# Optimization experiments

Measured on AMD Instinct MI355X. Metric: run time of the kernel, lower is better.

Reference implementation:

```python
import jax, jax.numpy as jnp
import numpy as np

N = 50000
E = 800000
D = 128


def setup_inputs() -> dict:
    key = jax.random.key(0)
    ks = jax.random.split(key, 10)
    x = jax.random.normal(ks[0], (N, D), dtype=jnp.float32)
    edge_index = jax.random.randint(ks[1], (2, E), 0, N, dtype=jnp.int32)
    s = 1.0 / np.sqrt(D)
    W1 = jax.random.uniform(ks[2], (D, D), jnp.float32, -s, s)
    b1 = jnp.zeros((D,), jnp.float32)
    W2 = jax.random.uniform(ks[3], (D, D), jnp.float32, -s, s)
    b2 = jnp.zeros((D,), jnp.float32)
    Wt = jax.random.uniform(ks[4], (D, 1), jnp.float32, -s, s)
    bt = jnp.zeros((1,), jnp.float32)
    We = jax.random.uniform(ks[5], (D, 1), jnp.float32, -s, s)
    be = jnp.zeros((1,), jnp.float32)
    return {"x": x, "edge_index": edge_index, "W1": W1, "b1": b1,
            "W2": W2, "b2": b2, "Wt": Wt, "bt": bt, "We": We, "be": be}


def _gcn_norm(edge_index, n):
    # add self-loops, then symmetric normalization D^-1/2 (A+I) D^-1/2
    loop = jnp.arange(n, dtype=edge_index.dtype)
    src = jnp.concatenate([edge_index[0], loop])
    dst = jnp.concatenate([edge_index[1], loop])
    ones = jnp.ones(src.shape[0], dtype=jnp.float32)
    deg = jax.ops.segment_sum(ones, dst, num_segments=n)
    dinv = jnp.where(deg > 0, jax.lax.rsqrt(deg), 0.0)
    norm = dinv[src] * dinv[dst]  # [E+N]
    return src, dst, norm


def _gcn_conv(h, W, b, src, dst, norm, n):
    h = h @ W                                   # [N, D'] dense GEMM
    msg = h[src] * norm[:, None]                # gather + scale
    out = jax.ops.segment_sum(msg, dst, num_segments=n)  # scatter-add
    return out + b


def reference(x, edge_index, W1, b1, W2, b2, Wt, bt, We, be):
    n = x.shape[0]
    src, dst, norm = _gcn_norm(edge_index, n)
    h = jax.nn.relu(_gcn_conv(x, W1, b1, src, dst, norm, n))
    h = jax.nn.relu(_gcn_conv(h, W2, b2, src, dst, norm, n))
    # dropout is identity at inference (eval mode)
    survival_time = h @ Wt + bt   # [N, 1]
    event_status = h @ We + be    # [N, 1]
    return survival_time, event_status
```

## Files before the change

kernel.cpp:

```cpp
#include <hip/hip_runtime.h>
#include <hip/hip_fp16.h>
#include <math.h>

#define NN 50000
#define NE 800000
#define DD 128

#define NB  196
#define CAP 5300
#define EPB 4096
#define A_BLOCKS 196

#define SLAB2 (NN * 64)

typedef _Float16 half8_t __attribute__((ext_vector_type(8)));
typedef float f32x4 __attribute__((ext_vector_type(4)));


__global__ __launch_bounds__(256) void k_setup(const int* __restrict__ src, const int* __restrict__ dst,
                                               int* __restrict__ bcnt, unsigned int* __restrict__ ebuf,
                                               const float* __restrict__ W1, const float* __restrict__ W2,
                                               __half* __restrict__ WT1, __half* __restrict__ WT2) {
    const int blk = blockIdx.x;
    const int tid = threadIdx.x;

    if (blk < A_BLOCKS) {
        __shared__ int hist[256];
        __shared__ int scanbuf[256];
        __shared__ int gbase[256];
        __shared__ unsigned int stage[EPB];
        __shared__ int tgt[EPB];

        const int e0 = blk * EPB;
        int nE = NE - e0; if (nE > EPB) nE = EPB;

        hist[tid] = 0;
        __syncthreads();

        unsigned int pk[16];
        unsigned int br[16];
        #pragma unroll
        for (int j = 0; j < 16; ++j) {
            int idx = tid + j * 256;
            if (idx < nE) {
                int e = e0 + idx;
                int s = src[e], d = dst[e];
                int b = d >> 8;
                int r = atomicAdd(&hist[b], 1);
                pk[j] = (unsigned int)s | ((unsigned int)(d & 255) << 16);
                br[j] = (unsigned int)b | ((unsigned int)r << 8);
            }
        }
        __syncthreads();
        int v = hist[tid];
        scanbuf[tid] = v;
        __syncthreads();
        for (int o = 1; o < 256; o <<= 1) {
            int t2 = (tid >= o) ? scanbuf[tid - o] : 0;
            __syncthreads();
            scanbuf[tid] += t2;
            __syncthreads();
        }
        int base_excl = scanbuf[tid] - v;
        if (tid < NB && v > 0) gbase[tid] = tid * CAP + atomicAdd(&bcnt[tid], v);
        hist[tid] = base_excl;
        __syncthreads();

        #pragma unroll
        for (int j = 0; j < 16; ++j) {
            int idx = tid + j * 256;
            if (idx < nE) {
                int b = br[j] & 255;
                int r = (int)(br[j] >> 8);
                int pos = hist[b] + r;
                stage[pos] = pk[j];
                tgt[pos]   = gbase[b] + r;
            }
        }
        __syncthreads();
        #pragma unroll
        for (int j = 0; j < 16; ++j) {
            int idx = tid + j * 256;
            if (idx < nE) ebuf[tgt[idx]] = stage[idx];
        }
    } else {
        const float* W  = (blk == A_BLOCKS) ? W1 : W2;
        __half*      WT = (blk == A_BLOCKS) ? WT1 : WT2;
        int n = tid >> 1;
        int k0 = (tid & 1) * 64;
        #pragma unroll 8
        for (int j = 0; j < 64; ++j) {
            int k = k0 + j;
            WT[n * DD + k] = __float2half(W[k * DD + n]);
        }
    }
}


__global__ __launch_bounds__(512) void k_build_csr(const unsigned int* __restrict__ ebuf,
                                                   const int* __restrict__ bcnt,
                                                   int* __restrict__ row_ptr,
                                                   float* __restrict__ dinv,
                                                   unsigned short* __restrict__ col) {
    __shared__ int cnt[256];
    __shared__ int scanb[256];
    __shared__ unsigned short stage[CAP];

    const int b   = blockIdx.x;
    const int tid = threadIdx.x;
    const int seg0 = b * CAP;
    const int sb   = bcnt[b];
    const int n0   = b << 8;
    int nb = NN - n0; if (nb > 256) nb = 256;

    if (tid < 256) scanb[tid] = (tid < NB) ? bcnt[tid] : 0;
    __syncthreads();
    for (int o = 1; o < 256; o <<= 1) {
        int t = 0;
        if (tid < 256 && tid >= o) t = scanb[tid - o];
        __syncthreads();
        if (tid < 256) scanb[tid] += t;
        __syncthreads();
    }
    const int rbase = scanb[b] - sb;
    __syncthreads();

    if (tid < 256) cnt[tid] = 0;
    __syncthreads();
    for (int p = tid; p < sb; p += 512) {
        unsigned int e = ebuf[seg0 + p];
        atomicAdd(&cnt[(e >> 16) & 255], 1);
    }
    __syncthreads();
    int v = (tid < 256) ? cnt[tid] : 0;
    if (tid < 256) scanb[tid] = v;
    __syncthreads();
    for (int o = 1; o < 256; o <<= 1) {
        int t = 0;
        if (tid < 256 && tid >= o) t = scanb[tid - o];
        __syncthreads();
        if (tid < 256) scanb[tid] += t;
        __syncthreads();
    }
    int excl = (tid < 256) ? (scanb[tid] - v) : 0;
    if (tid < nb) {
        row_ptr[n0 + tid] = rbase + excl;
        dinv[n0 + tid] = rsqrtf(1.0f + (float)v);
    }
    if (b == 0 && tid == 0) row_ptr[NN] = NE;
    if (tid < 256) cnt[tid] = excl;
    __syncthreads();
    for (int p = tid; p < sb; p += 512) {
        unsigned int e = ebuf[seg0 + p];
        int pos = atomicAdd(&cnt[(e >> 16) & 255], 1);
        stage[pos] = (unsigned short)(e & 0xFFFFu);
    }
    __syncthreads();
    for (int p = tid; p < sb; p += 512) {
        col[rbase + p] = stage[p];
    }
}


#define LPAD 136
#define GEMM_B 782
#define ZERO_B 98

__global__ __launch_bounds__(256) void k_gemm_x(const float* __restrict__ X, const __half* __restrict__ WT,
                                                const float* __restrict__ dinv, __half* __restrict__ Gc,
                                                float* __restrict__ zbuf, int zcount) {
    const int tid = threadIdx.x;

    if (blockIdx.x >= GEMM_B) {
        int idx = (blockIdx.x - GEMM_B) * 256 + tid;
        if (idx * 4 + 3 < zcount) ((float4*)zbuf)[idx] = make_float4(0.f, 0.f, 0.f, 0.f);
        else {
            for (int k = idx * 4; k < zcount; ++k) zbuf[k] = 0.f;
        }
        return;
    }

    __shared__ __half Wl[DD * LPAD];
    __shared__ __half Al[64 * LPAD];

    const int row0 = blockIdx.x * 64;

    {
        const uint4* WTg = (const uint4*)WT;
        #pragma unroll
        for (int j = 0; j < 8; ++j) {
            int u = tid + j * 256;
            int n = u >> 4, koff = (u & 15) * 8;
            uint4 v = WTg[u];
            *(uint4*)&Wl[n * LPAD + koff] = v;
        }
    }
    {
        const float4* X4 = (const float4*)X;
        #pragma unroll
        for (int j = 0; j < 8; ++j) {
            int u = tid + j * 256;
            int r = u >> 5, c4 = u & 31;
            int grow = row0 + r;
            float4 v = make_float4(0.f, 0.f, 0.f, 0.f);
            if (grow < NN) v = X4[(size_t)grow * 32 + c4];
            __half2 a = __floats2half2_rn(v.x, v.y);
            __half2 b = __floats2half2_rn(v.z, v.w);
            uint2 pk;
            pk.x = *(unsigned int*)&a;
            pk.y = *(unsigned int*)&b;
            *(uint2*)&Al[r * LPAD + c4 * 4] = pk;
        }
    }
    __syncthreads();

    const int wave = tid >> 6;
    const int lane = tid & 63;
    const int m    = lane & 15;
    const int quad = lane >> 4;

    f32x4 acc[8];
    #pragma unroll
    for (int t = 0; t < 8; ++t) acc[t] = (f32x4){0.f, 0.f, 0.f, 0.f};

    #pragma unroll
    for (int kk = 0; kk < DD; kk += 32) {
        half8_t a = *(const half8_t*)&Al[(wave * 16 + m) * LPAD + kk + quad * 8];
        #pragma unroll
        for (int t = 0; t < 8; ++t) {
            half8_t b = *(const half8_t*)&Wl[(t * 16 + m) * LPAD + kk + quad * 8];
            acc[t] = __builtin_amdgcn_mfma_f32_16x16x32_f16(a, b, acc[t], 0, 0, 0);
        }
    }

    __syncthreads();

    float4 dv = *(const float4*)&dinv[row0 + wave * 16 + quad * 4];

    #pragma unroll
    for (int t = 0; t < 8; ++t) {
        #pragma unroll
        for (int r = 0; r < 4; ++r) {
            int row_l = wave * 16 + quad * 4 + r;
            int c     = t * 16 + m;
            float val = acc[t][r] * ((const float*)&dv)[r];
            Al[row_l * LPAD + c] = __float2half(val);
        }
    }
    __syncthreads();

    {
        #pragma unroll
        for (int j = 0; j < 4; ++j) {
            int u = tid + j * 256;
            int r = u >> 4, c16 = u & 15;
            int ch = c16 >> 3, wi = c16 & 7;
            int grow = row0 + r;
            if (grow < NN) {
                uint4 v = *(const uint4*)&Al[r * LPAD + c16 * 8];
                *(uint4*)(Gc + (size_t)ch * SLAB2 + (size_t)grow * 64 + wi * 8) = v;
            }
        }
    }
}


__global__ __launch_bounds__(256) void k_gemm_h(const __half* __restrict__ Xc, const __half* __restrict__ WT,
                                                const float* __restrict__ dinv, __half* __restrict__ Gc) {
    __shared__ __half Wl[DD * LPAD];
    __shared__ __half Al[64 * LPAD];

    const int tid  = threadIdx.x;
    const int row0 = blockIdx.x * 64;

    {
        const uint4* WTg = (const uint4*)WT;
        #pragma unroll
        for (int j = 0; j < 8; ++j) {
            int u = tid + j * 256;
            int n = u >> 4, koff = (u & 15) * 8;
            uint4 v = WTg[u];
            *(uint4*)&Wl[n * LPAD + koff] = v;
        }
    }
    {
        #pragma unroll
        for (int j = 0; j < 4; ++j) {
            int u = tid + j * 256;
            int r = u >> 4, c16 = u & 15;
            int ch = c16 >> 3, wi = c16 & 7;
            int grow = row0 + r;
            uint4 v;
            if (grow < NN) v = *(const uint4*)(Xc + (size_t)ch * SLAB2 + (size_t)grow * 64 + wi * 8);
            else { v.x = 0; v.y = 0; v.z = 0; v.w = 0; }
            *(uint4*)&Al[r * LPAD + c16 * 8] = v;
        }
    }
    __syncthreads();

    const int wave = tid >> 6;
    const int lane = tid & 63;
    const int m    = lane & 15;
    const int quad = lane >> 4;

    f32x4 acc[8];
    #pragma unroll
    for (int t = 0; t < 8; ++t) acc[t] = (f32x4){0.f, 0.f, 0.f, 0.f};

    #pragma unroll
    for (int kk = 0; kk < DD; kk += 32) {
        half8_t a = *(const half8_t*)&Al[(wave * 16 + m) * LPAD + kk + quad * 8];
        #pragma unroll
        for (int t = 0; t < 8; ++t) {
            half8_t b = *(const half8_t*)&Wl[(t * 16 + m) * LPAD + kk + quad * 8];
            acc[t] = __builtin_amdgcn_mfma_f32_16x16x32_f16(a, b, acc[t], 0, 0, 0);
        }
    }

    __syncthreads();

    float4 dv = *(const float4*)&dinv[row0 + wave * 16 + quad * 4];

    #pragma unroll
    for (int t = 0; t < 8; ++t) {
        #pragma unroll
        for (int r = 0; r < 4; ++r) {
            int row_l = wave * 16 + quad * 4 + r;
            int c     = t * 16 + m;
            float val = acc[t][r] * ((const float*)&dv)[r];
            Al[row_l * LPAD + c] = __float2half(val);
        }
    }
    __syncthreads();

    {
        #pragma unroll
        for (int j = 0; j < 4; ++j) {
            int u = tid + j * 256;
            int r = u >> 4, c16 = u & 15;
            int ch = c16 >> 3, wi = c16 & 7;
            int grow = row0 + r;
            if (grow < NN) {
                uint4 v = *(const uint4*)&Al[r * LPAD + c16 * 8];
                *(uint4*)(Gc + (size_t)ch * SLAB2 + (size_t)grow * 64 + wi * 8) = v;
            }
        }
    }
}


__device__ inline float4 h4_to_f4(uint2 r) {
    __half2 a = *(__half2*)&r.x;
    __half2 b = *(__half2*)&r.y;
    float2 lo = __half22float2(a), hi = __half22float2(b);
    return make_float4(lo.x, lo.y, hi.x, hi.y);
}

__device__ inline uint2 f4_to_h4(float4 v) {
    __half2 a = __floats2half2_rn(v.x, v.y);
    __half2 b = __floats2half2_rn(v.z, v.w);
    uint2 r;
    r.x = *(unsigned int*)&a;
    r.y = *(unsigned int*)&b;
    return r;
}

__device__ inline float4 gather_grp64(const __half* __restrict__ slab, int node, int fl,
                                      const unsigned short* __restrict__ col, int beg, int end) {
    const __half* base = slab + fl * 4;
    float4 accA = h4_to_f4(*(const uint2*)(base + (size_t)node * 64));
    float4 accB = make_float4(0.f, 0.f, 0.f, 0.f);
    int p = beg;
    for (; p + 3 < end; p += 4) {
        int s0 = col[p], s1 = col[p + 1], s2 = col[p + 2], s3 = col[p + 3];
        float4 v0 = h4_to_f4(*(const uint2*)(base + (size_t)s0 * 64));
        float4 v1 = h4_to_f4(*(const uint2*)(base + (size_t)s1 * 64));
        float4 v2 = h4_to_f4(*(const uint2*)(base + (size_t)s2 * 64));
        float4 v3 = h4_to_f4(*(const uint2*)(base + (size_t)s3 * 64));
        accA.x += v0.x + v1.x; accA.y += v0.y + v1.y; accA.z += v0.z + v1.z; accA.w += v0.w + v1.w;
        accB.x += v2.x + v3.x; accB.y += v2.y + v3.y; accB.z += v2.z + v3.z; accB.w += v2.w + v3.w;
    }
    for (; p < end; ++p) {
        int s0 = col[p];
        float4 v0 = h4_to_f4(*(const uint2*)(base + (size_t)s0 * 64));
        accA.x += v0.x; accA.y += v0.y; accA.z += v0.z; accA.w += v0.w;
    }
    accA.x += accB.x; accA.y += accB.y; accA.z += accB.z; accA.w += accB.w;
    return accA;
}

__global__ __launch_bounds__(256) void k_aggregate_c(const __half* __restrict__ G, const float* __restrict__ dinv,
                                                     const int* __restrict__ row_ptr, const unsigned short* __restrict__ col,
                                                     const float* __restrict__ bias, __half* __restrict__ H) {
    const int bx    = blockIdx.x;
    const int slot  = bx & 7;
    const int chunk = slot >> 2;
    const int nb    = (bx >> 3) * 4 + (slot & 3);
    const int g     = threadIdx.x >> 4;
    const int fl    = threadIdx.x & 15;
    const int node  = nb * 16 + g;
    if (node >= NN) return;

    const __half* slab = G + (size_t)chunk * SLAB2;
    int beg = row_ptr[node];
    int end = row_ptr[node + 1];
    float4 acc = gather_grp64(slab, node, fl, col, beg, end);

    float di = dinv[node];
    float4 bv = *(const float4*)(bias + chunk * 64 + fl * 4);
    float4 hv;
    hv.x = fmaxf(fmaf(di, acc.x, bv.x), 0.f);
    hv.y = fmaxf(fmaf(di, acc.y, bv.y), 0.f);
    hv.z = fmaxf(fmaf(di, acc.z, bv.z), 0.f);
    hv.w = fmaxf(fmaf(di, acc.w, bv.w), 0.f);
    *(uint2*)(H + (size_t)chunk * SLAB2 + (size_t)node * 64 + fl * 4) = f4_to_h4(hv);
}

__global__ __launch_bounds__(256) void k_aggregate_heads_c(const __half* __restrict__ G, const float* __restrict__ dinv,
                                                           const int* __restrict__ row_ptr, const unsigned short* __restrict__ col,
                                                           const float* __restrict__ bias,
                                                           const float* __restrict__ Wt, const float* __restrict__ bt,
                                                           const float* __restrict__ We, const float* __restrict__ be,
                                                           float* __restrict__ out) {
    const int bx    = blockIdx.x;
    const int slot  = bx & 7;
    const int chunk = slot >> 2;
    const int nb    = (bx >> 3) * 4 + (slot & 3);
    const int g     = threadIdx.x >> 4;
    const int fl    = threadIdx.x & 15;
    const int node  = nb * 16 + g;
    if (node >= NN) return;

    const __half* slab = G + (size_t)chunk * SLAB2;
    int beg = row_ptr[node];
    int end = row_ptr[node + 1];
    float4 acc = gather_grp64(slab, node, fl, col, beg, end);

    float di = dinv[node];
    float4 bv = *(const float4*)(bias + chunk * 64 + fl * 4);
    float hx = fmaxf(fmaf(di, acc.x, bv.x), 0.f);
    float hy = fmaxf(fmaf(di, acc.y, bv.y), 0.f);
    float hz = fmaxf(fmaf(di, acc.z, bv.z), 0.f);
    float hw = fmaxf(fmaf(di, acc.w, bv.w), 0.f);

    float4 wt = *(const float4*)(Wt + chunk * 64 + fl * 4);
    float4 we = *(const float4*)(We + chunk * 64 + fl * 4);
    float t  = hx * wt.x + hy * wt.y + hz * wt.z + hw * wt.w;
    float ev = hx * we.x + hy * we.y + hz * we.z + hw * we.w;
    #pragma unroll
    for (int o = 1; o < 16; o <<= 1) {
        t  += __shfl_xor(t, o, 64);
        ev += __shfl_xor(ev, o, 64);
    }
    if (fl == 0) {
        if (chunk == 0) { t += bt[0]; ev += be[0]; }
        atomicAdd(&out[node], t);
        atomicAdd(&out[NN + node], ev);
    }
}


extern "C" void kernel_launch(void* const* d_in, const int* in_sizes, int n_in,
                              void* d_out, int out_size, void* d_ws, size_t ws_size,
                              hipStream_t stream) {
    const float* x  = (const float*)d_in[0];
    const int*   ei = (const int*)d_in[1];
    const float* W1 = (const float*)d_in[2];
    const float* b1 = (const float*)d_in[3];
    const float* W2 = (const float*)d_in[4];
    const float* b2 = (const float*)d_in[5];
    const float* Wt = (const float*)d_in[6];
    const float* bt = (const float*)d_in[7];
    const float* We = (const float*)d_in[8];
    const float* be = (const float*)d_in[9];
    float* out = (float*)d_out;

    const int* srcI = ei;
    const int* dstI = ei + NE;

    char* w = (char*)d_ws;
    __half*         Gh    = (__half*)w;         w += (size_t)NN * DD * sizeof(__half);
    __half*         H1h   = (__half*)w;         w += (size_t)NN * DD * sizeof(__half);
    __half*         WT1   = (__half*)w;         w += (size_t)DD * DD * sizeof(__half);
    __half*         WT2   = (__half*)w;         w += (size_t)DD * DD * sizeof(__half);
    unsigned int*   ebuf  = (unsigned int*)w;   w += (size_t)NB * CAP * sizeof(unsigned int);
    unsigned short* col   = (unsigned short*)w; w += (size_t)NE * sizeof(unsigned short);
    float*          dinv  = (float*)w;          w += (size_t)(NN + 64) * sizeof(float);
    int*            rowp  = (int*)w;            w += (size_t)(NN + 1) * sizeof(int);
    int*            bcnt  = (int*)w;            w += (size_t)NB * sizeof(int);

    const int SETUP_B = A_BLOCKS + 2;
    const int NBLK    = (NN + 15) / 16;
    const int AGG_B   = ((NBLK + 3) / 4) * 8;

    hipMemsetAsync(bcnt, 0, (size_t)NB * sizeof(int), stream);

    hipLaunchKernelGGL(k_setup,     dim3(SETUP_B), dim3(256), 0, stream,
                       srcI, dstI, bcnt, ebuf, W1, W2, WT1, WT2);
    hipLaunchKernelGGL(k_build_csr, dim3(NB),      dim3(512), 0, stream, ebuf, bcnt, rowp, dinv, col);

    hipLaunchKernelGGL(k_gemm_x,      dim3(GEMM_B + ZERO_B), dim3(256), 0, stream, x, WT1, dinv, Gh, out, out_size);
    hipLaunchKernelGGL(k_aggregate_c, dim3(AGG_B),           dim3(256), 0, stream, Gh, dinv, rowp, col, b1, H1h);

    hipLaunchKernelGGL(k_gemm_h,            dim3(GEMM_B), dim3(256), 0, stream, H1h, WT2, dinv, Gh);
    hipLaunchKernelGGL(k_aggregate_heads_c, dim3(AGG_B),  dim3(256), 0, stream, Gh, dinv, rowp, col, b2,
                       Wt, bt, We, be, out);
}
```

Before: 201.6 us.

## Fuse edge bucketing with first GEMM and move source-degree scaling into gather

The edge bucketing, the first dense GEMM (with an in-kernel W1 transpose) and the output zeroing are merged into one front kernel, so the GEMM no longer waits for the CSR build and the memset plus one launch go away. Because the GEMM now runs before dinv exists, the source-side D^-1/2 scaling moves out of the GEMM epilogue into the aggregation gather, which reads dinv per neighbor. The global atomic bucket counters are replaced by per-block count and offset tables, and the CSR kernel sums and scans these to assemble each bucket. The cost is an extra dinv load per edge in both aggregations, repeated W transposes in every GEMM block, and a serial per-thread copy loop in the CSR kernel.

```diff
diff --git a/kernel.cpp b/kernel.cpp
--- a/kernel.cpp
+++ b/kernel.cpp
@@ -10,26 +10,33 @@
 #define CAP 5300
 #define EPB 4096
 #define A_BLOCKS 196
+#define GEMM_B 782
+#define ZERO_B 98
+#define LPAD 136
+#define CSTRIDE 256
 
 #define SLAB2 (NN * 64)
+
+#define FRONT_SMEM (DD * LPAD * 2 + 64 * LPAD * 2)
 
 typedef _Float16 half8_t __attribute__((ext_vector_type(8)));
 typedef float f32x4 __attribute__((ext_vector_type(4)));
 
 
-__global__ __launch_bounds__(256) void k_setup(const int* __restrict__ src, const int* __restrict__ dst,
-                                               int* __restrict__ bcnt, unsigned int* __restrict__ ebuf,
-                                               const float* __restrict__ W1, const float* __restrict__ W2,
-                                               __half* __restrict__ WT1, __half* __restrict__ WT2) {
+__global__ __launch_bounds__(256) void k_front(const int* __restrict__ src, const int* __restrict__ dst,
+                                               unsigned int* __restrict__ ebuf2,
+                                               int* __restrict__ cnts_g, int* __restrict__ offs_g,
+                                               const float* __restrict__ X, const float* __restrict__ W1,
+                                               __half* __restrict__ G1,
+                                               float* __restrict__ outz, int zcount) {
+    __shared__ __align__(16) char smem[FRONT_SMEM];
     const int blk = blockIdx.x;
     const int tid = threadIdx.x;
 
     if (blk < A_BLOCKS) {
-        __shared__ int hist[256];
-        __shared__ int scanbuf[256];
-        __shared__ int gbase[256];
-        __shared__ unsigned int stage[EPB];
-        __shared__ int tgt[EPB];
+        int* hist          = (int*)smem;
+        int* scanbuf       = hist + 256;
+        unsigned int* stage = (unsigned int*)(smem + 2048);
 
         const int e0 = blk * EPB;
         int nE = NE - e0; if (nE > EPB) nE = EPB;
@@ -62,7 +69,10 @@
             __syncthreads();
         }
         int base_excl = scanbuf[tid] - v;
-        if (tid < NB && v > 0) gbase[tid] = tid * CAP + atomicAdd(&bcnt[tid], v);
+        if (tid < NB) {
+            cnts_g[blk * CSTRIDE + tid] = v;
+            offs_g[blk * CSTRIDE + tid] = base_excl;
+        }
         hist[tid] = base_excl;
         __syncthreads();
 
@@ -72,184 +82,83 @@
             if (idx < nE) {
                 int b = br[j] & 255;
                 int r = (int)(br[j] >> 8);
-                int pos = hist[b] + r;
-                stage[pos] = pk[j];
-                tgt[pos]   = gbase[b] + r;
+                stage[hist[b] + r] = pk[j];
             }
         }
         __syncthreads();
         #pragma unroll
         for (int j = 0; j < 16; ++j) {
             int idx = tid + j * 256;
-            if (idx < nE) ebuf[tgt[idx]] = stage[idx];
-        }
-    } else {
-        const float* W  = (blk == A_BLOCKS) ? W1 : W2;
-        __half*      WT = (blk == A_BLOCKS) ? WT1 : WT2;
-        int n = tid >> 1;
-        int k0 = (tid & 1) * 64;
-        #pragma unroll 8
-        for (int j = 0; j < 64; ++j) {
-            int k = k0 + j;
-            WT[n * DD + k] = __float2half(W[k * DD + n]);
-        }
-    }
-}
-
-
-__global__ __launch_bounds__(512) void k_build_csr(const unsigned int* __restrict__ ebuf,
-                                                   const int* __restrict__ bcnt,
-                                                   int* __restrict__ row_ptr,
-                                                   float* __restrict__ dinv,
-                                                   unsigned short* __restrict__ col) {
-    __shared__ int cnt[256];
-    __shared__ int scanb[256];
-    __shared__ unsigned short stage[CAP];
-
-    const int b   = blockIdx.x;
-    const int tid = threadIdx.x;
-    const int seg0 = b * CAP;
-    const int sb   = bcnt[b];
-    const int n0   = b << 8;
-    int nb = NN - n0; if (nb > 256) nb = 256;
-
-    if (tid < 256) scanb[tid] = (tid < NB) ? bcnt[tid] : 0;
-    __syncthreads();
-    for (int o = 1; o < 256; o <<= 1) {
-        int t = 0;
-        if (tid < 256 && tid >= o) t = scanb[tid - o];
-        __syncthreads();
-        if (tid < 256) scanb[tid] += t;
-        __syncthreads();
-    }
-    const int rbase = scanb[b] - sb;
-    __syncthreads();
-
-    if (tid < 256) cnt[tid] = 0;
-    __syncthreads();
-    for (int p = tid; p < sb; p += 512) {
-        unsigned int e = ebuf[seg0 + p];
-        atomicAdd(&cnt[(e >> 16) & 255], 1);
-    }
-    __syncthreads();
-    int v = (tid < 256) ? cnt[tid] : 0;
-    if (tid < 256) scanb[tid] = v;
-    __syncthreads();
-    for (int o = 1; o < 256; o <<= 1) {
-        int t = 0;
-        if (tid < 256 && tid >= o) t = scanb[tid - o];
-        __syncthreads();
-        if (tid < 256) scanb[tid] += t;
-        __syncthreads();
-    }
-    int excl = (tid < 256) ? (scanb[tid] - v) : 0;
-    if (tid < nb) {
-        row_ptr[n0 + tid] = rbase + excl;
-        dinv[n0 + tid] = rsqrtf(1.0f + (float)v);
-    }
-    if (b == 0 && tid == 0) row_ptr[NN] = NE;
-    if (tid < 256) cnt[tid] = excl;
-    __syncthreads();
-    for (int p = tid; p < sb; p += 512) {
-        unsigned int e = ebuf[seg0 + p];
-        int pos = atomicAdd(&cnt[(e >> 16) & 255], 1);
-        stage[pos] = (unsigned short)(e & 0xFFFFu);
-    }
-    __syncthreads();
-    for (int p = tid; p < sb; p += 512) {
-        col[rbase + p] = stage[p];
-    }
-}
-
-
-#define LPAD 136
-#define GEMM_B 782
-#define ZERO_B 98
-
-__global__ __launch_bounds__(256) void k_gemm_x(const float* __restrict__ X, const __half* __restrict__ WT,
-                                                const float* __restrict__ dinv, __half* __restrict__ Gc,
-                                                float* __restrict__ zbuf, int zcount) {
-    const int tid = threadIdx.x;
-
-    if (blockIdx.x >= GEMM_B) {
-        int idx = (blockIdx.x - GEMM_B) * 256 + tid;
-        if (idx * 4 + 3 < zcount) ((float4*)zbuf)[idx] = make_float4(0.f, 0.f, 0.f, 0.f);
-        else {
-            for (int k = idx * 4; k < zcount; ++k) zbuf[k] = 0.f;
-        }
-        return;
-    }
-
-    __shared__ __half Wl[DD * LPAD];
-    __shared__ __half Al[64 * LPAD];
-
-    const int row0 = blockIdx.x * 64;
-
-    {
-        const uint4* WTg = (const uint4*)WT;
-        #pragma unroll
-        for (int j = 0; j < 8; ++j) {
-            int u = tid + j * 256;
-            int n = u >> 4, koff = (u & 15) * 8;
-            uint4 v = WTg[u];
-            *(uint4*)&Wl[n * LPAD + koff] = v;
-        }
-    }
-    {
-        const float4* X4 = (const float4*)X;
-        #pragma unroll
-        for (int j = 0; j < 8; ++j) {
-            int u = tid + j * 256;
-            int r = u >> 5, c4 = u & 31;
-            int grow = row0 + r;
-            float4 v = make_float4(0.f, 0.f, 0.f, 0.f);
-            if (grow < NN) v = X4[(size_t)grow * 32 + c4];
-            __half2 a = __floats2half2_rn(v.x, v.y);
-            __half2 b = __floats2half2_rn(v.z, v.w);
-            uint2 pk;
-            pk.x = *(unsigned int*)&a;
-            pk.y = *(unsigned int*)&b;
-            *(uint2*)&Al[r * LPAD + c4 * 4] = pk;
-        }
-    }
-    __syncthreads();
-
-    const int wave = tid >> 6;
-    const int lane = tid & 63;
-    const int m    = lane & 15;
-    const int quad = lane >> 4;
-
-    f32x4 acc[8];
-    #pragma unroll
-    for (int t = 0; t < 8; ++t) acc[t] = (f32x4){0.f, 0.f, 0.f, 0.f};
-
-    #pragma unroll
-    for (int kk = 0; kk < DD; kk += 32) {
-        half8_t a = *(const half8_t*)&Al[(wave * 16 + m) * LPAD + kk + quad * 8];
+            if (idx < nE) ebuf2[(size_t)blk * EPB + idx] = stage[idx];
+        }
+    } else if (blk < A_BLOCKS + GEMM_B) {
+        __half* Wl = (__half*)smem;
+        __half* Al = (__half*)(smem + DD * LPAD * 2);
+        const int row0 = (blk - A_BLOCKS) * 64;
+
+        {
+            const float4* W4 = (const float4*)W1;
+            #pragma unroll
+            for (int j = 0; j < 16; ++j) {
+                int u = tid + j * 256;
+                int k = u >> 5, n4 = (u & 31) * 4;
+                float4 wv = W4[u];
+                Wl[(n4 + 0) * LPAD + k] = __float2half(wv.x);
+                Wl[(n4 + 1) * LPAD + k] = __float2half(wv.y);
+                Wl[(n4 + 2) * LPAD + k] = __float2half(wv.z);
+                Wl[(n4 + 3) * LPAD + k] = __float2half(wv.w);
+            }
+        }
+        {
+            const float4* X4 = (const float4*)X;
+            #pragma unroll
+            for (int j = 0; j < 8; ++j) {
+                int u = tid + j * 256;
+                int r = u >> 5, c4 = u & 31;
+                int grow = row0 + r;
+                float4 v = make_float4(0.f, 0.f, 0.f, 0.f);
+                if (grow < NN) v = X4[(size_t)grow * 32 + c4];
+                __half2 a = __floats2half2_rn(v.x, v.y);
+                __half2 b = __floats2half2_rn(v.z, v.w);
+                uint2 pkk;
+                pkk.x = *(unsigned int*)&a;
+                pkk.y = *(unsigned int*)&b;
+                *(uint2*)&Al[r * LPAD + c4 * 4] = pkk;
+            }
+        }
+        __syncthreads();
+
+        const int wave = tid >> 6;
+        const int lane = tid & 63;
+        const int m    = lane & 15;
+        const int quad = lane >> 4;
+
+        f32x4 acc[8];
+        #pragma unroll
+        for (int t = 0; t < 8; ++t) acc[t] = (f32x4){0.f, 0.f, 0.f, 0.f};
+
+        #pragma unroll
+        for (int kk = 0; kk < DD; kk += 32) {
+            half8_t a = *(const half8_t*)&Al[(wave * 16 + m) * LPAD + kk + quad * 8];
+            #pragma unroll
+            for (int t = 0; t < 8; ++t) {
+                half8_t b = *(const half8_t*)&Wl[(t * 16 + m) * LPAD + kk + quad * 8];
+                acc[t] = __builtin_amdgcn_mfma_f32_16x16x32_f16(a, b, acc[t], 0, 0, 0);
+            }
+        }
+        __syncthreads();
+
         #pragma unroll
         for (int t = 0; t < 8; ++t) {
-            half8_t b = *(const half8_t*)&Wl[(t * 16 + m) * LPAD + kk + quad * 8];
-            acc[t] = __builtin_amdgcn_mfma_f32_16x16x32_f16(a, b, acc[t], 0, 0, 0);
-        }
-    }
-
-    __syncthreads();
-
-    float4 dv = *(const float4*)&dinv[row0 + wave * 16 + quad * 4];
-
-    #pragma unroll
-    for (int t = 0; t < 8; ++t) {
-        #pragma unroll
-        for (int r = 0; r < 4; ++r) {
-            int row_l = wave * 16 + quad * 4 + r;
-            int c     = t * 16 + m;
-            float val = acc[t][r] * ((const float*)&dv)[r];
-            Al[row_l * LPAD + c] = __float2half(val);
-        }
-    }
-    __syncthreads();
-
-    {
+            #pragma unroll
+            for (int r = 0; r < 4; ++r) {
+                int row_l = wave * 16 + quad * 4 + r;
+                int c     = t * 16 + m;
+                Al[row_l * LPAD + c] = __float2half(acc[t][r]);
+            }
+        }
+        __syncthreads();
+
         #pragma unroll
         for (int j = 0; j < 4; ++j) {
             int u = tid + j * 256;
@@ -258,15 +167,117 @@
             int grow = row0 + r;
             if (grow < NN) {
                 uint4 v = *(const uint4*)&Al[r * LPAD + c16 * 8];
-                *(uint4*)(Gc + (size_t)ch * SLAB2 + (size_t)grow * 64 + wi * 8) = v;
-            }
-        }
-    }
-}
-
-
-__global__ __launch_bounds__(256) void k_gemm_h(const __half* __restrict__ Xc, const __half* __restrict__ WT,
-                                                const float* __restrict__ dinv, __half* __restrict__ Gc) {
+                *(uint4*)(G1 + (size_t)ch * SLAB2 + (size_t)grow * 64 + wi * 8) = v;
+            }
+        }
+    } else {
+        int idx = (blk - A_BLOCKS - GEMM_B) * 256 + tid;
+        if (idx * 4 + 3 < zcount) ((float4*)outz)[idx] = make_float4(0.f, 0.f, 0.f, 0.f);
+        else {
+            for (int k = idx * 4; k < zcount; ++k) outz[k] = 0.f;
+        }
+    }
+}
+
+
+__global__ __launch_bounds__(512) void k_csr(const unsigned int* __restrict__ ebuf2,
+                                             const int* __restrict__ cnts_g, const int* __restrict__ offs_g,
+                                             int* __restrict__ row_ptr, float* __restrict__ dinv,
+                                             unsigned short* __restrict__ col) {
+    __shared__ int colcnt[256];
+    __shared__ int runoff[256];
+    __shared__ int sizes[256];
+    __shared__ int cnt[256];
+    __shared__ int scanb[256];
+    __shared__ unsigned int stage32[CAP];
+    __shared__ unsigned short colst[CAP];
+
+    const int b   = blockIdx.x;
+    const int tid = threadIdx.x;
+    const int n0  = b << 8;
+    int nb = NN - n0; if (nb > 256) nb = 256;
+
+    if (tid < 256) {
+        int s = 0;
+        if (tid < NB) {
+            for (int k = 0; k < NB; ++k) s += cnts_g[k * CSTRIDE + tid];
+        }
+        sizes[tid]  = s;
+        colcnt[tid] = (tid < NB) ? cnts_g[tid * CSTRIDE + b] : 0;
+    }
+    __syncthreads();
+    const int sb = sizes[b];
+
+    if (tid < 256) scanb[tid] = sizes[tid];
+    __syncthreads();
+    for (int o = 1; o < 256; o <<= 1) {
+        int t = 0;
+        if (tid < 256 && tid >= o) t = scanb[tid - o];
+        __syncthreads();
+        if (tid < 256) scanb[tid] += t;
+        __syncthreads();
+    }
+    const int rbase = scanb[b] - sb;
+    __syncthreads();
+
+    if (tid < 256) scanb[tid] = colcnt[tid];
+    __syncthreads();
+    for (int o = 1; o < 256; o <<= 1) {
+        int t = 0;
+        if (tid < 256 && tid >= o) t = scanb[tid - o];
+        __syncthreads();
+        if (tid < 256) scanb[tid] += t;
+        __syncthreads();
+    }
+    if (tid < 256) runoff[tid] = scanb[tid] - colcnt[tid];
+    __syncthreads();
+
+    if (tid < NB) {
+        int len = colcnt[tid];
+        const unsigned int* s = ebuf2 + (size_t)tid * EPB + offs_g[tid * CSTRIDE + b];
+        unsigned int* d = stage32 + runoff[tid];
+        for (int i = 0; i < len; ++i) d[i] = s[i];
+    }
+    __syncthreads();
+
+    if (tid < 256) cnt[tid] = 0;
+    __syncthreads();
+    for (int p = tid; p < sb; p += 512) {
+        atomicAdd(&cnt[(stage32[p] >> 16) & 255], 1);
+    }
+    __syncthreads();
+    int v = (tid < 256) ? cnt[tid] : 0;
+    if (tid < 256) scanb[tid] = v;
+    __syncthreads();
+    for (int o = 1; o < 256; o <<= 1) {
+        int t = 0;
+        if (tid < 256 && tid >= o) t = scanb[tid - o];
+        __syncthreads();
+        if (tid < 256) scanb[tid] += t;
+        __syncthreads();
+    }
+    int excl = (tid < 256) ? (scanb[tid] - v) : 0;
+    if (tid < nb) {
+        row_ptr[n0 + tid] = rbase + excl;
+        dinv[n0 + tid] = rsqrtf(1.0f + (float)v);
+    }
+    if (b == 0 && tid == 0) row_ptr[NN] = NE;
+    if (tid < 256) cnt[tid] = excl;
+    __syncthreads();
+    for (int p = tid; p < sb; p += 512) {
+        unsigned int e = stage32[p];
+        int pos = atomicAdd(&cnt[(e >> 16) & 255], 1);
+        colst[pos] = (unsigned short)(e & 0xFFFFu);
+    }
+    __syncthreads();
+    for (int p = tid; p < sb; p += 512) {
+        col[rbase + p] = colst[p];
+    }
+}
+
+
+__global__ __launch_bounds__(256) void k_gemm2(const __half* __restrict__ Xc, const float* __restrict__ W2,
+                                               __half* __restrict__ Gc) {
     __shared__ __half Wl[DD * LPAD];
     __shared__ __half Al[64 * LPAD];
 
@@ -274,13 +285,16 @@
     const int row0 = blockIdx.x * 64;
 
     {
-        const uint4* WTg = (const uint4*)WT;
-        #pragma unroll
-        for (int j = 0; j < 8; ++j) {
+        const float4* W4 = (const float4*)W2;
+        #pragma unroll
+        for (int j = 0; j < 16; ++j) {
             int u = tid + j * 256;
-            int n = u >> 4, koff = (u & 15) * 8;
-            uint4 v = WTg[u];
-            *(uint4*)&Wl[n * LPAD + koff] = v;
+            int k = u >> 5, n4 = (u & 31) * 4;
+            float4 wv = W4[u];
+            Wl[(n4 + 0) * LPAD + k] = __float2half(wv.x);
+            Wl[(n4 + 1) * LPAD + k] = __float2half(wv.y);
+            Wl[(n4 + 2) * LPAD + k] = __float2half(wv.z);
+            Wl[(n4 + 3) * LPAD + k] = __float2half(wv.w);
         }
     }
     {
@@ -316,10 +330,7 @@
             acc[t] = __builtin_amdgcn_mfma_f32_16x16x32_f16(a, b, acc[t], 0, 0, 0);
         }
     }
-
-    __syncthreads();
-
-    float4 dv = *(const float4*)&dinv[row0 + wave * 16 + quad * 4];
+    __syncthreads();
 
     #pragma unroll
     for (int t = 0; t < 8; ++t) {
@@ -327,23 +338,20 @@
         for (int r = 0; r < 4; ++r) {
             int row_l = wave * 16 + quad * 4 + r;
             int c     = t * 16 + m;
-            float val = acc[t][r] * ((const float*)&dv)[r];
-            Al[row_l * LPAD + c] = __float2half(val);
-        }
-    }
-    __syncthreads();
-
-    {
-        #pragma unroll
-        for (int j = 0; j < 4; ++j) {
-            int u = tid + j * 256;
-            int r = u >> 4, c16 = u & 15;
-            int ch = c16 >> 3, wi = c16 & 7;
-            int grow = row0 + r;
-            if (grow < NN) {
-                uint4 v = *(const uint4*)&Al[r * LPAD + c16 * 8];
-                *(uint4*)(Gc + (size_t)ch * SLAB2 + (size_t)grow * 64 + wi * 8) = v;
-            }
+            Al[row_l * LPAD + c] = __float2half(acc[t][r]);
+        }
+    }
+    __syncthreads();
+
+    #pragma unroll
+    for (int j = 0; j < 4; ++j) {
+        int u = tid + j * 256;
+        int r = u >> 4, c16 = u & 15;
+        int ch = c16 >> 3, wi = c16 & 7;
+        int grow = row0 + r;
+        if (grow < NN) {
+            uint4 v = *(const uint4*)&Al[r * LPAD + c16 * 8];
+            *(uint4*)(Gc + (size_t)ch * SLAB2 + (size_t)grow * 64 + wi * 8) = v;
         }
     }
 }
@@ -365,25 +373,38 @@
     return r;
 }
 
-__device__ inline float4 gather_grp64(const __half* __restrict__ slab, int node, int fl,
+__device__ inline float4 gather_grp64(const __half* __restrict__ slab, const float* __restrict__ dinv,
+                                      float di, int node, int fl,
                                       const unsigned short* __restrict__ col, int beg, int end) {
     const __half* base = slab + fl * 4;
-    float4 accA = h4_to_f4(*(const uint2*)(base + (size_t)node * 64));
+    float4 sv = h4_to_f4(*(const uint2*)(base + (size_t)node * 64));
+    float4 accA = make_float4(di * sv.x, di * sv.y, di * sv.z, di * sv.w);
     float4 accB = make_float4(0.f, 0.f, 0.f, 0.f);
     int p = beg;
     for (; p + 3 < end; p += 4) {
         int s0 = col[p], s1 = col[p + 1], s2 = col[p + 2], s3 = col[p + 3];
+        float d0 = dinv[s0], d1 = dinv[s1], d2 = dinv[s2], d3 = dinv[s3];
         float4 v0 = h4_to_f4(*(const uint2*)(base + (size_t)s0 * 64));
         float4 v1 = h4_to_f4(*(const uint2*)(base + (size_t)s1 * 64));
         float4 v2 = h4_to_f4(*(const uint2*)(base + (size_t)s2 * 64));
         float4 v3 = h4_to_f4(*(const uint2*)(base + (size_t)s3 * 64));
-        accA.x += v0.x + v1.x; accA.y += v0.y + v1.y; accA.z += v0.z + v1.z; accA.w += v0.w + v1.w;
-        accB.x += v2.x + v3.x; accB.y += v2.y + v3.y; accB.z += v2.z + v3.z; accB.w += v2.w + v3.w;
+        accA.x = fmaf(d0, v0.x, fmaf(d1, v1.x, accA.x));
+        accA.y = fmaf(d0, v0.y, fmaf(d1, v1.y, accA.y));
+        accA.z = fmaf(d0, v0.z, fmaf(d1, v1.z, accA.z));
+        accA.w = fmaf(d0, v0.w, fmaf(d1, v1.w, accA.w));
+        accB.x = fmaf(d2, v2.x, fmaf(d3, v3.x, accB.x));
+        accB.y = fmaf(d2, v2.y, fmaf(d3, v3.y, accB.y));
+        accB.z = fmaf(d2, v2.z, fmaf(d3, v3.z, accB.z));
+        accB.w = fmaf(d2, v2.w, fmaf(d3, v3.w, accB.w));
     }
     for (; p < end; ++p) {
         int s0 = col[p];
+        float d0 = dinv[s0];
         float4 v0 = h4_to_f4(*(const uint2*)(base + (size_t)s0 * 64));
-        accA.x += v0.x; accA.y += v0.y; accA.z += v0.z; accA.w += v0.w;
+        accA.x = fmaf(d0, v0.x, accA.x);
+        accA.y = fmaf(d0, v0.y, accA.y);
+        accA.z = fmaf(d0, v0.z, accA.z);
+        accA.w = fmaf(d0, v0.w, accA.w);
     }
     accA.x += accB.x; accA.y += accB.y; accA.z += accB.z; accA.w += accB.w;
     return accA;
@@ -404,9 +425,9 @@
     const __half* slab = G + (size_t)chunk * SLAB2;
     int beg = row_ptr[node];
     int end = row_ptr[node + 1];
-    float4 acc = gather_grp64(slab, node, fl, col, beg, end);
-
     float di = dinv[node];
+    float4 acc = gather_grp64(slab, dinv, di, node, fl, col, beg, end);
+
     float4 bv = *(const float4*)(bias + chunk * 64 + fl * 4);
     float4 hv;
     hv.x = fmaxf(fmaf(di, acc.x, bv.x), 0.f);
@@ -434,9 +455,9 @@
     const __half* slab = G + (size_t)chunk * SLAB2;
     int beg = row_ptr[node];
     int end = row_ptr[node + 1];
-    float4 acc = gather_grp64(slab, node, fl, col, beg, end);
-
     float di = dinv[node];
+    float4 acc = gather_grp64(slab, dinv, di, node, fl, col, beg, end);
+
     float4 bv = *(const float4*)(bias + chunk * 64 + fl * 4);
     float hx = fmaxf(fmaf(di, acc.x, bv.x), 0.f);
     float hy = fmaxf(fmaf(di, acc.y, bv.y), 0.f);
@@ -481,28 +502,23 @@
     char* w = (char*)d_ws;
     __half*         Gh    = (__half*)w;         w += (size_t)NN * DD * sizeof(__half);
     __half*         H1h   = (__half*)w;         w += (size_t)NN * DD * sizeof(__half);
-    __half*         WT1   = (__half*)w;         w += (size_t)DD * DD * sizeof(__half);
-    __half*         WT2   = (__half*)w;         w += (size_t)DD * DD * sizeof(__half);
-    unsigned int*   ebuf  = (unsigned int*)w;   w += (size_t)NB * CAP * sizeof(unsigned int);
+    unsigned int*   ebuf2 = (unsigned int*)w;   w += (size_t)A_BLOCKS * EPB * sizeof(unsigned int);
     unsigned short* col   = (unsigned short*)w; w += (size_t)NE * sizeof(unsigned short);
     float*          dinv  = (float*)w;          w += (size_t)(NN + 64) * sizeof(float);
     int*            rowp  = (int*)w;            w += (size_t)(NN + 1) * sizeof(int);
-    int*            bcnt  = (int*)w;            w += (size_t)NB * sizeof(int);
-
-    const int SETUP_B = A_BLOCKS + 2;
+    int*            cnts  = (int*)w;            w += (size_t)A_BLOCKS * CSTRIDE * sizeof(int);
+    int*            offs  = (int*)w;            w += (size_t)A_BLOCKS * CSTRIDE * sizeof(int);
+
+    const int FRONT_B = A_BLOCKS + GEMM_B + ZERO_B;
     const int NBLK    = (NN + 15) / 16;
     const int AGG_B   = ((NBLK + 3) / 4) * 8;
 
-    hipMemsetAsync(bcnt, 0, (size_t)NB * sizeof(int), stream);
-
-    hipLaunchKernelGGL(k_setup,     dim3(SETUP_B), dim3(256), 0, stream,
-                       srcI, dstI, bcnt, ebuf, W1, W2, WT1, WT2);
-    hipLaunchKernelGGL(k_build_csr, dim3(NB),      dim3(512), 0, stream, ebuf, bcnt, rowp, dinv, col);
-
-    hipLaunchKernelGGL(k_gemm_x,      dim3(GEMM_B + ZERO_B), dim3(256), 0, stream, x, WT1, dinv, Gh, out, out_size);
-    hipLaunchKernelGGL(k_aggregate_c, dim3(AGG_B),           dim3(256), 0, stream, Gh, dinv, rowp, col, b1, H1h);
-
-    hipLaunchKernelGGL(k_gemm_h,            dim3(GEMM_B), dim3(256), 0, stream, H1h, WT2, dinv, Gh);
-    hipLaunchKernelGGL(k_aggregate_heads_c, dim3(AGG_B),  dim3(256), 0, stream, Gh, dinv, rowp, col, b2,
+    hipLaunchKernelGGL(k_front, dim3(FRONT_B), dim3(256), 0, stream,
+                       srcI, dstI, ebuf2, cnts, offs, x, W1, Gh, out, out_size);
+    hipLaunchKernelGGL(k_csr,   dim3(NB),      dim3(512), 0, stream, ebuf2, cnts, offs, rowp, dinv, col);
+
+    hipLaunchKernelGGL(k_aggregate_c, dim3(AGG_B), dim3(256), 0, stream, Gh, dinv, rowp, col, b1, H1h);
+    hipLaunchKernelGGL(k_gemm2,       dim3(GEMM_B), dim3(256), 0, stream, H1h, W2, Gh);
+    hipLaunchKernelGGL(k_aggregate_heads_c, dim3(AGG_B), dim3(256), 0, stream, Gh, dinv, rowp, col, b2,
                        Wt, bt, We, be, out);
 }
```

Measured after the change: 214.5 us. 6.4% more time.
